# Optimization experiments

Measured on AMD Instinct MI355X. Metric: run time of the kernel, lower is better.

## Reference

```python
import jax, jax.numpy as jnp
import numpy as np

B, S, D, H = 4, 2048, 768, 12
HD = D // H  # 64
ROPE_BASE = 10000.0


def setup_inputs() -> dict:
    key = jax.random.key(0)
    ks = jax.random.split(key, 9)
    sc = 1.0 / np.sqrt(D)
    return {
        "hidden_states": jax.random.normal(ks[0], (B, S, D), jnp.float32),
        "position_ids": jnp.broadcast_to(jnp.arange(S, dtype=jnp.int32)[None, :], (B, S)),
        "wq": jax.random.normal(ks[1], (D, D), jnp.float32) * sc,
        "bq": jax.random.normal(ks[2], (D,), jnp.float32) * 0.02,
        "wk": jax.random.normal(ks[3], (D, D), jnp.float32) * sc,
        "bk": jax.random.normal(ks[4], (D,), jnp.float32) * 0.02,
        "wv": jax.random.normal(ks[5], (D, D), jnp.float32) * sc,
        "bv": jax.random.normal(ks[6], (D,), jnp.float32) * 0.02,
        "wo": jax.random.normal(ks[7], (D, D), jnp.float32) * sc,
    }


def _rotate_half(x):
    x1, x2 = jnp.split(x, 2, axis=-1)
    return jnp.concatenate([-x2, x1], axis=-1)


def _rope_cos_sin(position_ids):
    # LLaMA-style rotary embedding: inv_freq over even dims, concat(freqs, freqs)
    inv_freq = 1.0 / (ROPE_BASE ** (jnp.arange(0, HD, 2, dtype=jnp.float32) / HD))  # [HD/2]
    freqs = position_ids.astype(jnp.float32)[:, :, None] * inv_freq[None, None, :]  # [B,S,HD/2]
    emb = jnp.concatenate([freqs, freqs], axis=-1)  # [B,S,HD]
    # add head-broadcast dim -> [B,1,S,HD]
    return jnp.cos(emb)[:, None], jnp.sin(emb)[:, None]


def reference(hidden_states, position_ids, wq, bq, wk, bk, wv, bv, wo):
    b, s, _ = hidden_states.shape
    # QKV projections (nn.Linear: x @ W.T + b), reshape to [B,H,S,HD]
    def proj(w, bias):
        y = jnp.einsum('bsd,ed->bse', hidden_states, w) + bias
        return y.reshape(b, s, H, HD).transpose(0, 2, 1, 3)

    q, k, v = proj(wq, bq), proj(wk, bk), proj(wv, bv)

    cos, sin = _rope_cos_sin(position_ids)
    q = q * cos + _rotate_half(q) * sin
    k = k * cos + _rotate_half(k) * sin

    # scaled dot-product attention (no mask, dropout_p=0 at eval)
    scores = jnp.einsum('bhqd,bhkd->bhqk', q, k) / jnp.sqrt(jnp.float32(HD))
    probs = jax.nn.softmax(scores, axis=-1)
    attn = jnp.einsum('bhqk,bhkd->bhqd', probs, v)

    attn = attn.transpose(0, 2, 1, 3).reshape(b, s, D)
    return jnp.einsum('bsd,ed->bse', attn, wo)
```

## Files before the change

kernel.cpp:

```cpp
#include <hip/hip_runtime.h>
#include <hip/hip_bf16.h>
#include <cstdint>
#include <cstddef>

#define B_ 4
#define S_ 2048
#define D_ 768
#define H_ 12
#define M_ 8192
#define KD 768

typedef unsigned short u16;
typedef __attribute__((ext_vector_type(8))) short short8;
typedef __attribute__((ext_vector_type(4))) short short4v;
typedef __attribute__((ext_vector_type(4))) float f32x4;
typedef __attribute__((ext_vector_type(16))) float f32x16;

static __device__ __forceinline__ u16 f2bf(float f) {
  union { float f; unsigned u; } x; x.f = f;
  unsigned r = x.u + 0x7fffu + ((x.u >> 16) & 1u);
  return (u16)(r >> 16);
}

static __device__ __forceinline__ unsigned cvtpk_bf16(float lo, float hi) {
  unsigned r;
  asm("v_cvt_pk_bf16_f32 %0, %1, %2" : "=v"(r) : "v"(lo), "v"(hi));
  return r;
}

static __device__ __forceinline__ void gload_lds16(const void* g, void* l) {
  __builtin_amdgcn_global_load_lds(
      (const __attribute__((address_space(1))) unsigned int*)g,
      (__attribute__((address_space(3))) unsigned int*)l,
      16, 0, 0);
}

__global__ __launch_bounds__(256) void cvt_kernel(const float* __restrict__ src,
                                                  u16* __restrict__ dst, int n8) {
  int i = blockIdx.x * 256 + threadIdx.x;
  if (i >= n8) return;
  const float4* s4p = (const float4*)src;
  float4 a = s4p[2 * i], b = s4p[2 * i + 1];
  short8 o;
  o[0] = (short)f2bf(a.x); o[1] = (short)f2bf(a.y);
  o[2] = (short)f2bf(a.z); o[3] = (short)f2bf(a.w);
  o[4] = (short)f2bf(b.x); o[5] = (short)f2bf(b.y);
  o[6] = (short)f2bf(b.z); o[7] = (short)f2bf(b.w);
  *(short8*)(dst + (size_t)i * 8) = o;
}

__global__ __launch_bounds__(256) void cvtw_kernel(const float* __restrict__ w0,
                                                   const float* __restrict__ w1,
                                                   const float* __restrict__ w2,
                                                   const float* __restrict__ w3,
                                                   u16* __restrict__ dst) {
  int z = blockIdx.y;
  const float* src = (z == 0) ? w0 : (z == 1) ? w1 : (z == 2) ? w2 : w3;
  int i = blockIdx.x * 256 + threadIdx.x;
  const float4* s4p = (const float4*)src;
  float4 a = s4p[2 * i], b = s4p[2 * i + 1];
  short8 o;
  o[0] = (short)f2bf(a.x); o[1] = (short)f2bf(a.y);
  o[2] = (short)f2bf(a.z); o[3] = (short)f2bf(a.w);
  o[4] = (short)f2bf(b.x); o[5] = (short)f2bf(b.y);
  o[6] = (short)f2bf(b.z); o[7] = (short)f2bf(b.w);
  *(short8*)(dst + (size_t)z * D_ * D_ + (size_t)i * 8) = o;
}

__global__ __launch_bounds__(256) void rope_table_kernel(const int* __restrict__ pos,
                                                         float* __restrict__ cost,
                                                         float* __restrict__ sint) {
  int idx = blockIdx.x * 256 + threadIdx.x;
  int j = idx & 31, ms = idx >> 5;
  float inv = exp2f(-(float)j * (13.287712379549449f / 32.0f));
  float th = (float)pos[ms] * inv;
  float s, c;
  sincosf(th, &s, &c);
  cost[idx] = c; sint[idx] = s;
}

__global__ __launch_bounds__(256, 2) void qkv_gemm_kernel(
    const u16* __restrict__ xbf, const u16* __restrict__ wbf,
    const float* __restrict__ bqp, const float* __restrict__ bkp, const float* __restrict__ bvp,
    const float* __restrict__ cost, const float* __restrict__ sint,
    u16* __restrict__ qbuf, u16* __restrict__ kbuf, u16* __restrict__ vtbuf) {
  __shared__ u16 lA[2][128][32];
  __shared__ u16 lB[2][128][32];
  const int z = blockIdx.z;
  const u16* wz = wbf + (size_t)z * (D_ * D_);
  const float* bias = (z == 0) ? bqp : (z == 1 ? bkp : bvp);
  const int m0 = blockIdx.y * 128;
  const int n0 = blockIdx.x * 128;
  const int t = threadIdx.x;
  const int lane = t & 63, l4 = lane >> 4, l15 = lane & 15;
  const int w = t >> 6, wm = w >> 1, wn = w & 1;

  f32x4 acc[4][4];
#pragma unroll
  for (int m = 0; m < 4; m++)
#pragma unroll
    for (int n = 0; n < 4; n++) acc[m][n] = (f32x4){0.f, 0.f, 0.f, 0.f};

  auto stage = [&](int buf, int k0) {
#pragma unroll
    for (int i = 0; i < 2; i++) {
      int slot = t + 256 * i;
      int row = slot >> 2;
      int s4 = (slot & 3) ^ ((row >> 1) & 3);
      gload_lds16(xbf + (size_t)(m0 + row) * KD + k0 + s4 * 8, &lA[buf][0][0] + slot * 8);
    }
#pragma unroll
    for (int i = 0; i < 2; i++) {
      int slot = t + 256 * i;
      int row = slot >> 2;
      int s4 = (slot & 3) ^ ((row >> 1) & 3);
      gload_lds16(wz + (size_t)(n0 + row) * KD + k0 + s4 * 8, &lB[buf][0][0] + slot * 8);
    }
  };

  stage(0, 0);
  int cur = 0;
  for (int kt = 0; kt < KD / 32; ++kt) {
    __syncthreads();
    if (kt + 1 < KD / 32) stage(cur ^ 1, (kt + 1) * 32);
    short8 af[4], bf[4];
#pragma unroll
    for (int m = 0; m < 4; m++) {
      int row = wm * 64 + m * 16 + l15;
      int s4 = l4 ^ ((row >> 1) & 3);
      af[m] = *(const short8*)(&lA[cur][row][s4 * 8]);
    }
#pragma unroll
    for (int n = 0; n < 4; n++) {
      int row = wn * 64 + n * 16 + l15;
      int s4 = l4 ^ ((row >> 1) & 3);
      bf[n] = *(const short8*)(&lB[cur][row][s4 * 8]);
    }
    __builtin_amdgcn_s_setprio(1);
#pragma unroll
    for (int m = 0; m < 4; m++)
#pragma unroll
      for (int n = 0; n < 4; n++)
        acc[m][n] = __builtin_amdgcn_mfma_f32_16x16x32_bf16(af[m], bf[n], acc[m][n], 0, 0, 0);
    __builtin_amdgcn_s_setprio(0);
    cur ^= 1;
  }

  const int mg_base = m0 + wm * 64;
  const int ng_base = n0 + wn * 64;
  const int h = ng_base >> 6;
  float bn[4];
#pragma unroll
  for (int n = 0; n < 4; n++) bn[n] = bias[ng_base + n * 16 + l15];

  if (z <= 1) {
    const float scale = (z == 0) ? 0.18033688011112042f : 1.0f;
    u16* dst = (z == 0) ? qbuf : kbuf;
#pragma unroll
    for (int m = 0; m < 4; m++) {
#pragma unroll
      for (int r = 0; r < 4; r++) {
        int mg = mg_base + m * 16 + (l4 << 2) + r;
        float c0 = cost[mg * 32 + l15],      s0 = sint[mg * 32 + l15];
        float c1 = cost[mg * 32 + 16 + l15], s1 = sint[mg * 32 + 16 + l15];
        float a0 = acc[m][0][r] + bn[0];
        float a1 = acc[m][1][r] + bn[1];
        float a2 = acc[m][2][r] + bn[2];
        float a3 = acc[m][3][r] + bn[3];
        float o0 = a0 * c0 - a2 * s0;
        float o1 = a1 * c1 - a3 * s1;
        float o2 = a2 * c0 + a0 * s0;
        float o3 = a3 * c1 + a1 * s1;
        int bb = mg >> 11, ss = mg & (S_ - 1);
        size_t rowoff = ((size_t)(bb * H_ + h) * S_ + ss) * 64;
        dst[rowoff + l15]      = f2bf(o0 * scale);
        dst[rowoff + 16 + l15] = f2bf(o1 * scale);
        dst[rowoff + 32 + l15] = f2bf(o2 * scale);
        dst[rowoff + 48 + l15] = f2bf(o3 * scale);
      }
    }
  } else {
#pragma unroll
    for (int m = 0; m < 4; m++) {
      int mgb = mg_base + m * 16 + (l4 << 2);
      int bb = mgb >> 11, ss = mgb & (S_ - 1);
#pragma unroll
      for (int n = 0; n < 4; n++) {
        int hd = n * 16 + l15;
        short4v o;
#pragma unroll
        for (int r = 0; r < 4; r++) o[r] = (short)f2bf(acc[m][n][r] + bn[n]);
        *(short4v*)(vtbuf + ((size_t)(bb * H_ + h) * 64 + hd) * S_ + ss) = o;
      }
    }
  }
}

__global__ __launch_bounds__(256, 4) void attn_kernel(const u16* __restrict__ qbuf,
                                                      const u16* __restrict__ kbuf,
                                                      const u16* __restrict__ vtbuf,
                                                      u16* __restrict__ abuf) {
  __shared__ u16 kt_[2][64][64];
  const int bh = blockIdx.x;
  const int b = bh / H_, h = bh % H_;
  const int t = threadIdx.x, lane = t & 63;
  const int w = t >> 6;
  const int l31 = lane & 31, hi = lane >> 5;
  const int q = blockIdx.y * 128 + w * 32 + l31;
  const u16* qb = qbuf + (size_t)bh * S_ * 64;
  const u16* kb = kbuf + (size_t)bh * S_ * 64;
  const u16* vb = vtbuf + (size_t)bh * 64 * S_;

  short8 qf[4];
#pragma unroll
  for (int ks = 0; ks < 4; ks++)
    qf[ks] = *(const short8*)(qb + (size_t)q * 64 + ks * 16 + hi * 8);

  f32x16 oacc[2];
#pragma unroll
  for (int r = 0; r < 16; r++) { oacc[0][r] = 0.f; oacc[1][r] = 0.f; }
  float mrun = -3.0e38f, lrun = 0.f;

  auto stageK = [&](int buf, int kv0) {
#pragma unroll
    for (int i = 0; i < 2; i++) {
      int slot = t + 256 * i;
      int row = slot >> 3;
      int s8 = (slot & 7) ^ (row & 7);
      gload_lds16(kb + (size_t)(kv0 + row) * 64 + s8 * 8, &kt_[buf][0][0] + slot * 8);
    }
  };

  stageK(0, 0);
  __syncthreads();

  const int NT = S_ / 64;
  for (int t_ = 0; t_ < NT; ++t_) {
    const int kv0 = t_ * 64, buf = t_ & 1;
    if (t_ + 1 < NT) stageK(buf ^ 1, kv0 + 64);

#pragma unroll
    for (int sub = 0; sub < 2; ++sub) {
      const int kvs = sub * 32;
      short8 vf[2][2];
#pragma unroll
      for (int hh = 0; hh < 2; hh++)
#pragma unroll
        for (int kt2 = 0; kt2 < 2; kt2++)
          vf[hh][kt2] = *(const short8*)(vb + (size_t)(hh * 32 + l31) * S_ +
                                         kv0 + kvs + kt2 * 16 + hi * 8);

      f32x16 sacc;
#pragma unroll
      for (int r = 0; r < 16; r++) sacc[r] = 0.f;
      const char* kbase = (const char*)&kt_[buf][0][0];
      __builtin_amdgcn_s_setprio(1);
#pragma unroll
      for (int ks = 0; ks < 4; ks++) {
        int row = kvs + l31;
        int byte = ((ks * 2 + hi) * 16) ^ ((row & 7) << 4);
        short8 kf = *(const short8*)(kbase + row * 128 + byte);
        sacc = __builtin_amdgcn_mfma_f32_32x32x16_bf16(kf, qf[ks], sacc, 0, 0, 0);
      }
      __builtin_amdgcn_s_setprio(0);

      float mx = sacc[0];
#pragma unroll
      for (int r = 1; r < 16; r++) mx = fmaxf(mx, sacc[r]);
      mx = fmaxf(mx, __shfl_xor(mx, 32));
      bool ok = (mx <= mrun + 11.0f);
      if (!__all((int)ok)) {
        float nm = fmaxf(mrun, mx);
        float al = exp2f(mrun - nm);
        lrun *= al;
#pragma unroll
        for (int r = 0; r < 16; r++) { oacc[0][r] *= al; oacc[1][r] *= al; }
        mrun = nm;
      }
      float p[16];
      float ls = 0.f;
#pragma unroll
      for (int r = 0; r < 16; r++) { p[r] = exp2f(sacc[r] - mrun); ls += p[r]; }
      ls += __shfl_xor(ls, 32);
      lrun += ls;

      unsigned a0 = cvtpk_bf16(p[0], p[1]),   a1 = cvtpk_bf16(p[2], p[3]);
      unsigned b0 = cvtpk_bf16(p[4], p[5]),   b1 = cvtpk_bf16(p[6], p[7]);
      unsigned c0 = cvtpk_bf16(p[8], p[9]),   c1 = cvtpk_bf16(p[10], p[11]);
      unsigned d0 = cvtpk_bf16(p[12], p[13]), d1 = cvtpk_bf16(p[14], p[15]);
      unsigned xa0 = __shfl_xor(a0, 32), xa1 = __shfl_xor(a1, 32);
      unsigned xb0 = __shfl_xor(b0, 32), xb1 = __shfl_xor(b1, 32);
      unsigned xc0 = __shfl_xor(c0, 32), xc1 = __shfl_xor(c1, 32);
      unsigned xd0 = __shfl_xor(d0, 32), xd1 = __shfl_xor(d1, 32);
      union PW { unsigned w[4]; short8 s; };
      PW pw0, pw1;
      pw0.w[0] = hi ? xb0 : a0;  pw0.w[1] = hi ? xb1 : a1;
      pw0.w[2] = hi ? b0 : xa0;  pw0.w[3] = hi ? b1 : xa1;
      pw1.w[0] = hi ? xd0 : c0;  pw1.w[1] = hi ? xd1 : c1;
      pw1.w[2] = hi ? d0 : xc0;  pw1.w[3] = hi ? d1 : xc1;

      __builtin_amdgcn_s_setprio(1);
      oacc[0] = __builtin_amdgcn_mfma_f32_32x32x16_bf16(vf[0][0], pw0.s, oacc[0], 0, 0, 0);
      oacc[0] = __builtin_amdgcn_mfma_f32_32x32x16_bf16(vf[0][1], pw1.s, oacc[0], 0, 0, 0);
      oacc[1] = __builtin_amdgcn_mfma_f32_32x32x16_bf16(vf[1][0], pw0.s, oacc[1], 0, 0, 0);
      oacc[1] = __builtin_amdgcn_mfma_f32_32x32x16_bf16(vf[1][1], pw1.s, oacc[1], 0, 0, 0);
      __builtin_amdgcn_s_setprio(0);
    }
    __syncthreads();
  }

  float inv = 1.0f / lrun;
  u16* orow = abuf + (size_t)(b * S_ + q) * D_ + h * 64;
#pragma unroll
  for (int hh = 0; hh < 2; hh++)
#pragma unroll
    for (int i = 0; i < 8; i++) {
      int hd = ((2 * i) & 3) + 8 * (i >> 1) + 4 * hi + 32 * hh;
      unsigned pk = cvtpk_bf16(oacc[hh][2 * i] * inv, oacc[hh][2 * i + 1] * inv);
      *(unsigned*)(orow + hd) = pk;
    }
}

__global__ __launch_bounds__(256, 2) void out_gemm_kernel(const u16* __restrict__ abuf,
                                                          const u16* __restrict__ wobf,
                                                          float* __restrict__ out) {
  __shared__ u16 lA[2][128][32];
  __shared__ u16 lB[2][128][32];
  const int m0 = blockIdx.y * 128;
  const int n0 = blockIdx.x * 128;
  const int t = threadIdx.x;
  const int lane = t & 63, l4 = lane >> 4, l15 = lane & 15;
  const int w = t >> 6, wm = w >> 1, wn = w & 1;

  f32x4 acc[4][4];
#pragma unroll
  for (int m = 0; m < 4; m++)
#pragma unroll
    for (int n = 0; n < 4; n++) acc[m][n] = (f32x4){0.f, 0.f, 0.f, 0.f};

  auto stage = [&](int buf, int k0) {
#pragma unroll
    for (int i = 0; i < 2; i++) {
      int slot = t + 256 * i;
      int row = slot >> 2;
      int s4 = (slot & 3) ^ ((row >> 1) & 3);
      gload_lds16(abuf + (size_t)(m0 + row) * KD + k0 + s4 * 8, &lA[buf][0][0] + slot * 8);
    }
#pragma unroll
    for (int i = 0; i < 2; i++) {
      int slot = t + 256 * i;
      int row = slot >> 2;
      int s4 = (slot & 3) ^ ((row >> 1) & 3);
      gload_lds16(wobf + (size_t)(n0 + row) * KD + k0 + s4 * 8, &lB[buf][0][0] + slot * 8);
    }
  };

  stage(0, 0);
  int cur = 0;
  for (int kt = 0; kt < KD / 32; ++kt) {
    __syncthreads();
    if (kt + 1 < KD / 32) stage(cur ^ 1, (kt + 1) * 32);
    short8 af[4], bf[4];
#pragma unroll
    for (int m = 0; m < 4; m++) {
      int row = wm * 64 + m * 16 + l15;
      int s4 = l4 ^ ((row >> 1) & 3);
      af[m] = *(const short8*)(&lA[cur][row][s4 * 8]);
    }
#pragma unroll
    for (int n = 0; n < 4; n++) {
      int row = wn * 64 + n * 16 + l15;
      int s4 = l4 ^ ((row >> 1) & 3);
      bf[n] = *(const short8*)(&lB[cur][row][s4 * 8]);
    }
    __builtin_amdgcn_s_setprio(1);
#pragma unroll
    for (int m = 0; m < 4; m++)
#pragma unroll
      for (int n = 0; n < 4; n++)
        acc[m][n] = __builtin_amdgcn_mfma_f32_16x16x32_bf16(af[m], bf[n], acc[m][n], 0, 0, 0);
    __builtin_amdgcn_s_setprio(0);
    cur ^= 1;
  }

  const int mg_base = m0 + wm * 64;
  const int ng_base = n0 + wn * 64;
#pragma unroll
  for (int m = 0; m < 4; m++)
#pragma unroll
    for (int r = 0; r < 4; r++) {
      int mg = mg_base + m * 16 + (l4 << 2) + r;
      size_t rb = (size_t)mg * D_ + ng_base + l15;
      out[rb]      = acc[m][0][r];
      out[rb + 16] = acc[m][1][r];
      out[rb + 32] = acc[m][2][r];
      out[rb + 48] = acc[m][3][r];
    }
}

extern "C" void kernel_launch(void* const* d_in, const int* in_sizes, int n_in,
                              void* d_out, int out_size, void* d_ws, size_t ws_size,
                              hipStream_t stream) {
  const float* hs  = (const float*)d_in[0];
  const int*   pos = (const int*)d_in[1];
  const float* wq  = (const float*)d_in[2];
  const float* bq  = (const float*)d_in[3];
  const float* wk  = (const float*)d_in[4];
  const float* bk  = (const float*)d_in[5];
  const float* wv  = (const float*)d_in[6];
  const float* bv  = (const float*)d_in[7];
  const float* wo  = (const float*)d_in[8];
  float* out = (float*)d_out;

  u16* xbf   = (u16*)d_ws;
  u16* wbf   = xbf + (size_t)M_ * D_;
  u16* qbuf  = wbf + (size_t)4 * D_ * D_;
  u16* kbuf  = qbuf + (size_t)M_ * D_;
  u16* vtbuf = kbuf + (size_t)M_ * D_;
  u16* abuf  = vtbuf + (size_t)M_ * D_;
  float* cost = (float*)(abuf + (size_t)M_ * D_);
  float* sint = cost + (size_t)M_ * 32;

  cvt_kernel<<<dim3((M_ * D_ / 8 + 255) / 256), dim3(256), 0, stream>>>(hs, xbf, M_ * D_ / 8);
  cvtw_kernel<<<dim3(D_ * D_ / 8 / 256, 4), dim3(256), 0, stream>>>(wq, wk, wv, wo, wbf);

  rope_table_kernel<<<dim3(M_ * 32 / 256), dim3(256), 0, stream>>>(pos, cost, sint);

  qkv_gemm_kernel<<<dim3(D_ / 128, M_ / 128, 3), dim3(256), 0, stream>>>(
      xbf, wbf, bq, bk, bv, cost, sint, qbuf, kbuf, vtbuf);

  attn_kernel<<<dim3(B_ * H_, S_ / 128), dim3(256), 0, stream>>>(qbuf, kbuf, vtbuf, abuf);

  out_gemm_kernel<<<dim3(D_ / 128, M_ / 128), dim3(256), 0, stream>>>(abuf, wbf + (size_t)3 * D_ * D_, out);
}
```

Before: 268.5 us.

## Load K directly to registers, use permlane32 swap and MFMA row-sum in attention

Drops the LDS double-buffered K staging and the per-tile barrier in the attention kernel. Each wave now loads its K fragments straight from global memory into registers. The P-matrix lane exchange uses v_permlane32_swap in place of shuffles plus selects. The softmax denominator is accumulated with extra MFMAs against a ones vector instead of a VALU sum and shuffle, and the max reduction uses three-way fmax. Occupancy hint lowered to 3 blocks per SM, which trades register budget for occupancy and adds redundant global K traffic across the 4 waves of a block.

```diff
diff --git a/kernel.cpp b/kernel.cpp
--- a/kernel.cpp
+++ b/kernel.cpp
@@ -26,6 +26,14 @@
   unsigned r;
   asm("v_cvt_pk_bf16_f32 %0, %1, %2" : "=v"(r) : "v"(lo), "v"(hi));
   return r;
+}
+
+static __device__ __forceinline__ void plane32_swap(unsigned& a, unsigned& b) {
+  asm("v_permlane32_swap_b32 %0, %1" : "+v"(a), "+v"(b));
+}
+
+static __device__ __forceinline__ float fmax3(float a, float b, float c) {
+  return fmaxf(fmaxf(a, b), c);
 }
 
 static __device__ __forceinline__ void gload_lds16(const void* g, void* l) {
@@ -196,11 +204,10 @@
   }
 }
 
-__global__ __launch_bounds__(256, 4) void attn_kernel(const u16* __restrict__ qbuf,
+__global__ __launch_bounds__(256, 3) void attn_kernel(const u16* __restrict__ qbuf,
                                                       const u16* __restrict__ kbuf,
                                                       const u16* __restrict__ vtbuf,
                                                       u16* __restrict__ abuf) {
-  __shared__ u16 kt_[2][64][64];
   const int bh = blockIdx.x;
   const int b = bh / H_, h = bh % H_;
   const int t = threadIdx.x, lane = t & 63;
@@ -208,108 +215,100 @@
   const int l31 = lane & 31, hi = lane >> 5;
   const int q = blockIdx.y * 128 + w * 32 + l31;
   const u16* qb = qbuf + (size_t)bh * S_ * 64;
-  const u16* kb = kbuf + (size_t)bh * S_ * 64;
-  const u16* vb = vtbuf + (size_t)bh * 64 * S_;
+  const char* kb = (const char*)(kbuf + (size_t)bh * S_ * 64);
+  const char* vb = (const char*)(vtbuf + (size_t)bh * 64 * S_);
 
   short8 qf[4];
 #pragma unroll
   for (int ks = 0; ks < 4; ks++)
     qf[ks] = *(const short8*)(qb + (size_t)q * 64 + ks * 16 + hi * 8);
 
-  f32x16 oacc[2];
-#pragma unroll
-  for (int r = 0; r < 16; r++) { oacc[0][r] = 0.f; oacc[1][r] = 0.f; }
-  float mrun = -3.0e38f, lrun = 0.f;
-
-  auto stageK = [&](int buf, int kv0) {
-#pragma unroll
-    for (int i = 0; i < 2; i++) {
-      int slot = t + 256 * i;
-      int row = slot >> 3;
-      int s8 = (slot & 7) ^ (row & 7);
-      gload_lds16(kb + (size_t)(kv0 + row) * 64 + s8 * 8, &kt_[buf][0][0] + slot * 8);
-    }
-  };
-
-  stageK(0, 0);
-  __syncthreads();
+  short8 ones;
+#pragma unroll
+  for (int i = 0; i < 8; i++) ones[i] = (short)0x3F80;
+
+  f32x16 oacc[2], lacc;
+#pragma unroll
+  for (int r = 0; r < 16; r++) { oacc[0][r] = 0.f; oacc[1][r] = 0.f; lacc[r] = 0.f; }
+  float mrun = -3.0e38f;
+
+  const int kvo = l31 * 128 + hi * 16;
+  const int vvo0 = l31 * 4096 + hi * 16;
+  const int vvo1 = (32 + l31) * 4096 + hi * 16;
 
   const int NT = S_ / 64;
   for (int t_ = 0; t_ < NT; ++t_) {
-    const int kv0 = t_ * 64, buf = t_ & 1;
-    if (t_ + 1 < NT) stageK(buf ^ 1, kv0 + 64);
+    const int kbase = t_ * 8192;
+    short8 kf[2][4];
+#pragma unroll
+    for (int sub = 0; sub < 2; sub++)
+#pragma unroll
+      for (int ks = 0; ks < 4; ks++)
+        kf[sub][ks] = *(const short8*)(kb + kbase + sub * 4096 + kvo + ks * 32);
 
 #pragma unroll
     for (int sub = 0; sub < 2; ++sub) {
-      const int kvs = sub * 32;
+      const int vbase = t_ * 128 + sub * 64;
       short8 vf[2][2];
 #pragma unroll
-      for (int hh = 0; hh < 2; hh++)
-#pragma unroll
-        for (int kt2 = 0; kt2 < 2; kt2++)
-          vf[hh][kt2] = *(const short8*)(vb + (size_t)(hh * 32 + l31) * S_ +
-                                         kv0 + kvs + kt2 * 16 + hi * 8);
+      for (int kt2 = 0; kt2 < 2; kt2++) {
+        vf[0][kt2] = *(const short8*)(vb + vvo0 + vbase + kt2 * 32);
+        vf[1][kt2] = *(const short8*)(vb + vvo1 + vbase + kt2 * 32);
+      }
 
       f32x16 sacc;
 #pragma unroll
       for (int r = 0; r < 16; r++) sacc[r] = 0.f;
-      const char* kbase = (const char*)&kt_[buf][0][0];
       __builtin_amdgcn_s_setprio(1);
 #pragma unroll
-      for (int ks = 0; ks < 4; ks++) {
-        int row = kvs + l31;
-        int byte = ((ks * 2 + hi) * 16) ^ ((row & 7) << 4);
-        short8 kf = *(const short8*)(kbase + row * 128 + byte);
-        sacc = __builtin_amdgcn_mfma_f32_32x32x16_bf16(kf, qf[ks], sacc, 0, 0, 0);
-      }
+      for (int ks = 0; ks < 4; ks++)
+        sacc = __builtin_amdgcn_mfma_f32_32x32x16_bf16(kf[sub][ks], qf[ks], sacc, 0, 0, 0);
       __builtin_amdgcn_s_setprio(0);
 
-      float mx = sacc[0];
-#pragma unroll
-      for (int r = 1; r < 16; r++) mx = fmaxf(mx, sacc[r]);
+      float m0 = fmax3(sacc[0], sacc[1], sacc[2]);
+      float m1 = fmax3(sacc[3], sacc[4], sacc[5]);
+      float m2 = fmax3(sacc[6], sacc[7], sacc[8]);
+      float m3 = fmax3(sacc[9], sacc[10], sacc[11]);
+      float m4 = fmax3(sacc[12], sacc[13], sacc[14]);
+      float mx = fmaxf(fmax3(fmax3(m0, m1, m2), m3, m4), sacc[15]);
       mx = fmaxf(mx, __shfl_xor(mx, 32));
-      bool ok = (mx <= mrun + 11.0f);
-      if (!__all((int)ok)) {
+      if (!__all((int)(mx <= mrun + 11.0f))) {
         float nm = fmaxf(mrun, mx);
         float al = exp2f(mrun - nm);
-        lrun *= al;
 #pragma unroll
         for (int r = 0; r < 16; r++) { oacc[0][r] *= al; oacc[1][r] *= al; }
+        lacc[0] *= al;
         mrun = nm;
       }
       float p[16];
-      float ls = 0.f;
-#pragma unroll
-      for (int r = 0; r < 16; r++) { p[r] = exp2f(sacc[r] - mrun); ls += p[r]; }
-      ls += __shfl_xor(ls, 32);
-      lrun += ls;
+#pragma unroll
+      for (int r = 0; r < 16; r++) p[r] = exp2f(sacc[r] - mrun);
 
       unsigned a0 = cvtpk_bf16(p[0], p[1]),   a1 = cvtpk_bf16(p[2], p[3]);
       unsigned b0 = cvtpk_bf16(p[4], p[5]),   b1 = cvtpk_bf16(p[6], p[7]);
       unsigned c0 = cvtpk_bf16(p[8], p[9]),   c1 = cvtpk_bf16(p[10], p[11]);
       unsigned d0 = cvtpk_bf16(p[12], p[13]), d1 = cvtpk_bf16(p[14], p[15]);
-      unsigned xa0 = __shfl_xor(a0, 32), xa1 = __shfl_xor(a1, 32);
-      unsigned xb0 = __shfl_xor(b0, 32), xb1 = __shfl_xor(b1, 32);
-      unsigned xc0 = __shfl_xor(c0, 32), xc1 = __shfl_xor(c1, 32);
-      unsigned xd0 = __shfl_xor(d0, 32), xd1 = __shfl_xor(d1, 32);
+      plane32_swap(a0, b0);
+      plane32_swap(a1, b1);
+      plane32_swap(c0, d0);
+      plane32_swap(c1, d1);
       union PW { unsigned w[4]; short8 s; };
       PW pw0, pw1;
-      pw0.w[0] = hi ? xb0 : a0;  pw0.w[1] = hi ? xb1 : a1;
-      pw0.w[2] = hi ? b0 : xa0;  pw0.w[3] = hi ? b1 : xa1;
-      pw1.w[0] = hi ? xd0 : c0;  pw1.w[1] = hi ? xd1 : c1;
-      pw1.w[2] = hi ? d0 : xc0;  pw1.w[3] = hi ? d1 : xc1;
+      pw0.w[0] = a0; pw0.w[1] = a1; pw0.w[2] = b0; pw0.w[3] = b1;
+      pw1.w[0] = c0; pw1.w[1] = c1; pw1.w[2] = d0; pw1.w[3] = d1;
 
       __builtin_amdgcn_s_setprio(1);
       oacc[0] = __builtin_amdgcn_mfma_f32_32x32x16_bf16(vf[0][0], pw0.s, oacc[0], 0, 0, 0);
       oacc[0] = __builtin_amdgcn_mfma_f32_32x32x16_bf16(vf[0][1], pw1.s, oacc[0], 0, 0, 0);
       oacc[1] = __builtin_amdgcn_mfma_f32_32x32x16_bf16(vf[1][0], pw0.s, oacc[1], 0, 0, 0);
       oacc[1] = __builtin_amdgcn_mfma_f32_32x32x16_bf16(vf[1][1], pw1.s, oacc[1], 0, 0, 0);
+      lacc = __builtin_amdgcn_mfma_f32_32x32x16_bf16(ones, pw0.s, lacc, 0, 0, 0);
+      lacc = __builtin_amdgcn_mfma_f32_32x32x16_bf16(ones, pw1.s, lacc, 0, 0, 0);
       __builtin_amdgcn_s_setprio(0);
     }
-    __syncthreads();
   }
 
-  float inv = 1.0f / lrun;
+  float inv = 1.0f / lacc[0];
   u16* orow = abuf + (size_t)(b * S_ + q) * D_ + h * 64;
 #pragma unroll
   for (int hh = 0; hh < 2; hh++)
```

Measured after the change: 344.3 us. +28.2%, slower.
